# Kernel optimization log

Measured on AMD Instinct MI355X. Metric: run time of the kernel, lower is better.

The kernel has to match this reference:

```python
import jax, jax.numpy as jnp
import numpy as np

RADIUS, HMIN, HMAX, NSAMPLE = 0.05, -0.02, 0.04, 32
EPS = 1e-5


def setup_inputs() -> dict:
    key = jax.random.key(0)
    ks = jax.random.split(key, 6)
    B, N, C, OUT = 4, 2048, 256, 256
    seed_xyz_graspable = jax.random.uniform(ks[0], (B, N, 3), jnp.float32) * 0.2
    seed_features_graspable = jax.random.normal(ks[1], (B, C, N), jnp.float32)
    vp_rot = jax.random.normal(ks[2], (B, N, 3, 3), jnp.float32)
    W1 = jax.random.normal(ks[3], (OUT, 3 + C), jnp.float32) * 0.02
    W2 = jax.random.normal(ks[4], (OUT, OUT), jnp.float32) * 0.02
    return {
        "seed_xyz_graspable": seed_xyz_graspable,
        "seed_features_graspable": seed_features_graspable,
        "vp_rot": vp_rot,
        "W1": W1, "gamma1": jnp.ones((OUT,), jnp.float32), "beta1": jnp.zeros((OUT,), jnp.float32),
        "W2": W2, "gamma2": jnp.ones((OUT,), jnp.float32), "beta2": jnp.zeros((OUT,), jnp.float32),
    }


def _cylinder_query(xyz, rot):
    # xyz: (B,N,3), rot: (B,N,3,3); new_xyz == xyz.
    B, N, _ = xyz.shape
    d = xyz[:, None, :, :] - xyz[:, :, None, :]                  # (B,P,N,3) offsets to each candidate
    r = jnp.einsum('bpij,bpnj->bpni', rot, d)                    # rotate into cylinder frame (rot @ d)
    mask = (r[..., 1] ** 2 + r[..., 2] ** 2 < RADIUS ** 2) & (r[..., 0] > HMIN) & (r[..., 0] < HMAX)
    order = jnp.arange(N, dtype=jnp.int32)
    keys = jnp.where(mask, order, order + N)                     # in-cylinder points sort first, stable order
    _, idx = jax.lax.top_k(-keys, NSAMPLE)                       # first NSAMPLE indices satisfying the query
    valid = jnp.take_along_axis(mask, idx, axis=-1)
    first = idx[..., :1]
    any_valid = valid[..., :1]
    idx = jnp.where(valid, idx, jnp.where(any_valid, first, 0))  # pad with first hit like the CUDA kernel
    return idx                                                   # (B,P,NSAMPLE) int32


def _group(xyz, features, rot, idx):
    gxyz = jax.vmap(lambda a, i: a[i])(xyz, idx)                 # (B,P,S,3)
    gxyz = (gxyz - xyz[:, :, None, :]) / RADIUS                  # center on query + normalize_xyz
    gxyz = jnp.einsum('bpsj,bpjk->bpsk', gxyz, rot)              # rotate_xyz: grouped_xyz @ rot
    gfeat = jax.vmap(lambda f, i: f[:, i])(features, idx)        # (B,C,P,S)
    return jnp.concatenate([gxyz.transpose(0, 3, 1, 2), gfeat], axis=1)  # (B,3+C,P,S)


def _conv_bn_relu(x, W, gamma, beta):
    y = jnp.einsum('oc,bcps->bops', W, x)                        # 1x1 conv, no bias (bn=True)
    mu = y.mean(axis=(0, 2, 3), keepdims=True)
    var = y.var(axis=(0, 2, 3), keepdims=True)
    y = (y - mu) * jax.lax.rsqrt(var + EPS)
    y = y * gamma[None, :, None, None] + beta[None, :, None, None]
    return jax.nn.relu(y)


def reference(seed_xyz_graspable, seed_features_graspable, vp_rot, W1, gamma1, beta1, W2, gamma2, beta2):
    idx = _cylinder_query(seed_xyz_graspable, vp_rot)
    g = _group(seed_xyz_graspable, seed_features_graspable, vp_rot, idx)
    h = _conv_bn_relu(g, W1, gamma1, beta1)
    h = _conv_bn_relu(h, W2, gamma2, beta2)
    return h.max(axis=3)                                         # maxpool over nsample -> (B,OUT,P)
```

## Files before the change

kernel.cpp:

```cpp
#include <hip/hip_runtime.h>

typedef unsigned short u16;
typedef unsigned int u32;
typedef __attribute__((ext_vector_type(8))) short bf16x8;
typedef __attribute__((ext_vector_type(4))) float f32x4;

#define NPTS 2048
#define CFEAT 256
#define NS 32
#define MTOT 262144
#define NBLK 4096
#define INV_N (1.0f/262144.0f)

__device__ __forceinline__ float bf2f(u16 u) {
    union { u32 i; float f; } v; v.i = ((u32)u) << 16; return v.f;
}
__device__ __forceinline__ u16 f2bf(float f) {
    union { float f; u32 i; } v; v.f = f;
    u32 i = v.i;
    return (u16)((i + 0x7fffu + ((i >> 16) & 1u)) >> 16);
}

__global__ __launch_bounds__(256) void prep_k(const float* __restrict__ W1, const float* __restrict__ W2,
                                              u16* __restrict__ Wp1, u16* __restrict__ Wp2) {
    int o = blockIdx.x, t = threadIdx.x;
    Wp1[o * 288 + t] = f2bf(W1[o * 259 + 3 + t]);
    if (t < 32) Wp1[o * 288 + 256 + t] = (t < 3) ? f2bf(W1[o * 259 + t]) : (u16)0;
    Wp2[o * 256 + t] = f2bf(W2[o * 256 + t]);
}

__global__ __launch_bounds__(256) void query_k(const float* __restrict__ xyz, const float* __restrict__ rot,
                                               int* __restrict__ idx) {
    int pid = blockIdx.x * 4 + (threadIdx.x >> 6);
    int lane = threadIdx.x & 63;
    int b = pid >> 11, p = pid & 2047;
    const float* xb = xyz + (size_t)b * NPTS * 3;
    float px = xb[p * 3 + 0], py = xb[p * 3 + 1], pz = xb[p * 3 + 2];
    const float* rp = rot + (size_t)pid * 9;
    float r00 = rp[0], r01 = rp[1], r02 = rp[2];
    float r10 = rp[3], r11 = rp[4], r12 = rp[5];
    float r20 = rp[6], r21 = rp[7], r22 = rp[8];
    int cnt = 0, first = 0;
    for (int n0 = 0; n0 < NPTS && cnt < NS; n0 += 64) {
        int n = n0 + lane;
        float dx = __fsub_rn(xb[n * 3 + 0], px);
        float dy = __fsub_rn(xb[n * 3 + 1], py);
        float dz = __fsub_rn(xb[n * 3 + 2], pz);
        float a0 = __fadd_rn(__fadd_rn(__fmul_rn(r00, dx), __fmul_rn(r01, dy)), __fmul_rn(r02, dz));
        float a1 = __fadd_rn(__fadd_rn(__fmul_rn(r10, dx), __fmul_rn(r11, dy)), __fmul_rn(r12, dz));
        float a2 = __fadd_rn(__fadd_rn(__fmul_rn(r20, dx), __fmul_rn(r21, dy)), __fmul_rn(r22, dz));
        float t2 = __fadd_rn(__fmul_rn(a1, a1), __fmul_rn(a2, a2));
        bool valid = (t2 < 0.0025f) && (a0 > -0.02f) && (a0 < 0.04f);
        unsigned long long bal = __ballot(valid);
        if (cnt == 0 && bal) first = n0 + __builtin_ctzll(bal);
        int rank = __builtin_popcountll(bal & ((1ull << lane) - 1ull));
        int slot = cnt + rank;
        if (valid && slot < NS) idx[(size_t)pid * NS + slot] = n;
        cnt += __builtin_popcountll(bal);
    }
    int filled = cnt < NS ? cnt : NS;
    if (lane >= filled && lane < NS) idx[(size_t)pid * NS + lane] = (cnt > 0) ? first : 0;
}

__global__ __launch_bounds__(256) void featT_k(const float* __restrict__ feat, u16* __restrict__ featT) {
    __shared__ float sm[32 * 33];
    int b = blockIdx.z;
    int n0 = blockIdx.x * 32, c0 = blockIdx.y * 32;
    int t = threadIdx.x, x = t & 31, y = t >> 5;
    #pragma unroll
    for (int rr = 0; rr < 4; rr++) {
        int c = c0 + y + rr * 8;
        sm[(y + rr * 8) * 33 + x] = feat[((size_t)(b * CFEAT + c)) * NPTS + n0 + x];
    }
    __syncthreads();
    #pragma unroll
    for (int rr = 0; rr < 4; rr++) {
        int n = n0 + y + rr * 8;
        featT[((size_t)(b * NPTS + n)) * CFEAT + c0 + x] = f2bf(sm[x * 33 + (y + rr * 8)]);
    }
}

__global__ __launch_bounds__(256) void gxyz_k(const float* __restrict__ xyz, const float* __restrict__ rot,
                                              const int* __restrict__ idx, u16* __restrict__ gxyz) {
    int m = blockIdx.x * 256 + threadIdx.x;
    int pid = m >> 5;
    int b = pid >> 11, p = pid & 2047;
    int i = idx[m];
    const float* xb = xyz + (size_t)b * NPTS * 3;
    float dx = (xb[i * 3 + 0] - xb[p * 3 + 0]) * 20.0f;
    float dy = (xb[i * 3 + 1] - xb[p * 3 + 1]) * 20.0f;
    float dz = (xb[i * 3 + 2] - xb[p * 3 + 2]) * 20.0f;
    const float* rp = rot + (size_t)pid * 9;
    float g0 = dx * rp[0] + dy * rp[3] + dz * rp[6];
    float g1 = dx * rp[1] + dy * rp[4] + dz * rp[7];
    float g2 = dx * rp[2] + dy * rp[5] + dz * rp[8];
    uint2 v;
    v.x = (u32)f2bf(g0) | ((u32)f2bf(g1) << 16);
    v.y = (u32)f2bf(g2);
    *(uint2*)(gxyz + (size_t)m * 4) = v;
}

template <int FULL, int STORE>
__global__ __launch_bounds__(256) void fused_k(
    const u16* __restrict__ featT, const u16* __restrict__ gxyz, const int* __restrict__ idx,
    const u16* __restrict__ Wp1, const u16* __restrict__ Wp2, const float* __restrict__ ab1,
    float* __restrict__ psum, float* __restrict__ psq,
    float* __restrict__ ymax, float* __restrict__ ymin, uint2* __restrict__ y1f)
{
    __shared__ __attribute__((aligned(16))) u16 As[64 * 32];
    __shared__ __attribute__((aligned(16))) u16 Bs[256 * 32];
    __shared__ __attribute__((aligned(16))) u16 y1s[FULL ? 64 * 264 : 16];
    __shared__ int rowbase_s[64];

    const int tid = threadIdx.x;
    const int lane = tid & 63, wave = tid >> 6;
    const int quad = lane >> 4, tl = lane & 15;
    const int bx = blockIdx.x;
    const int m0 = bx * 64;

    if (tid < 64) {
        int m = m0 + tid;
        int gi = idx[m];
        int b = m >> 16;
        rowbase_s[tid] = (b * NPTS + gi) * CFEAT;
    }
    __syncthreads();
    const int srow = tid >> 2, sc16 = tid & 3;
    const int abase = rowbase_s[srow] + sc16 * 8;

    f32x4 acc[4][4];
    #pragma unroll
    for (int i = 0; i < 4; i++)
        #pragma unroll
        for (int j = 0; j < 4; j++) acc[i][j] = (f32x4){0.f, 0.f, 0.f, 0.f};

    auto mfma_tile = [&](f32x4 (&ac)[4][4], const u16* a_lds, int a_stride) {
        bf16x8 af[4], bv[4];
        #pragma unroll
        for (int i = 0; i < 4; i++) af[i] = *(const bf16x8*)(a_lds + (i * 16 + tl) * a_stride + quad * 8);
        #pragma unroll
        for (int j = 0; j < 4; j++) bv[j] = *(const bf16x8*)(Bs + (wave * 64 + j * 16 + tl) * 32 + quad * 8);
        #pragma unroll
        for (int i = 0; i < 4; i++)
            #pragma unroll
            for (int j = 0; j < 4; j++)
                ac[i][j] = __builtin_amdgcn_mfma_f32_16x16x32_bf16(af[i], bv[j], ac[i][j], 0, 0, 0);
    };

    for (int ks = 0; ks < 8; ks++) {
        const int k0 = ks * 32;
        __syncthreads();
        *(uint4*)(As + srow * 32 + sc16 * 8) = *(const uint4*)(featT + abase + k0);
        #pragma unroll
        for (int q = 0; q < 4; q++) {
            int o = srow + q * 64;
            *(uint4*)(Bs + o * 32 + sc16 * 8) = *(const uint4*)(Wp1 + o * 288 + k0 + sc16 * 8);
        }
        __syncthreads();
        mfma_tile(acc, As, 32);
    }
    {
        __syncthreads();
        uint4 va = make_uint4(0, 0, 0, 0);
        if (sc16 == 0) {
            uint2 g2 = *(const uint2*)(gxyz + (size_t)(m0 + srow) * 4);
            va.x = g2.x; va.y = g2.y;
        }
        *(uint4*)(As + srow * 32 + sc16 * 8) = va;
        #pragma unroll
        for (int q = 0; q < 4; q++) {
            int o = srow + q * 64;
            *(uint4*)(Bs + o * 32 + sc16 * 8) = *(const uint4*)(Wp1 + o * 288 + 256 + sc16 * 8);
        }
        __syncthreads();
        mfma_tile(acc, As, 32);
    }

    if (!FULL) {
        #pragma unroll
        for (int j = 0; j < 4; j++) {
            float s = 0.f, q2 = 0.f;
            #pragma unroll
            for (int i = 0; i < 4; i++) {
                float v0 = acc[i][j][0], v1 = acc[i][j][1], v2 = acc[i][j][2], v3 = acc[i][j][3];
                if (STORE) {
                    u32 lo = (u32)f2bf(v0) | ((u32)f2bf(v1) << 16);
                    u32 hi = (u32)f2bf(v2) | ((u32)f2bf(v3) << 16);
                    y1f[((size_t)(bx * 4 + wave) * 16 + i * 4 + j) * 64 + lane] = make_uint2(lo, hi);
                    v0 = bf2f((u16)(lo & 0xffff)); v1 = bf2f((u16)(lo >> 16));
                    v2 = bf2f((u16)(hi & 0xffff)); v3 = bf2f((u16)(hi >> 16));
                }
                s += v0 + v1 + v2 + v3;
                q2 += v0 * v0 + v1 * v1 + v2 * v2 + v3 * v3;
            }
            s += __shfl_xor(s, 16); s += __shfl_xor(s, 32);
            q2 += __shfl_xor(q2, 16); q2 += __shfl_xor(q2, 32);
            if (quad == 0) {
                int col = wave * 64 + j * 16 + tl;
                psum[(size_t)col * NBLK + bx] = s;
                psq[(size_t)col * NBLK + bx] = q2;
            }
        }
        return;
    }

    #pragma unroll
    for (int j = 0; j < 4; j++) {
        int col = wave * 64 + j * 16 + tl;
        float a = ab1[col], bb = ab1[256 + col];
        #pragma unroll
        for (int i = 0; i < 4; i++)
            #pragma unroll
            for (int r = 0; r < 4; r++) {
                float v = fmaxf(fmaf(acc[i][j][r], a, bb), 0.f);
                y1s[(i * 16 + quad * 4 + r) * 264 + col] = f2bf(v);
            }
    }

    f32x4 acc2[4][4];
    #pragma unroll
    for (int i = 0; i < 4; i++)
        #pragma unroll
        for (int j = 0; j < 4; j++) acc2[i][j] = (f32x4){0.f, 0.f, 0.f, 0.f};
    for (int ks = 0; ks < 8; ks++) {
        const int k0 = ks * 32;
        __syncthreads();
        #pragma unroll
        for (int q = 0; q < 4; q++) {
            int o = srow + q * 64;
            *(uint4*)(Bs + o * 32 + sc16 * 8) = *(const uint4*)(Wp2 + o * 256 + k0 + sc16 * 8);
        }
        __syncthreads();
        mfma_tile(acc2, y1s + k0, 264);
    }

    #pragma unroll
    for (int j = 0; j < 4; j++) {
        int col = wave * 64 + j * 16 + tl;
        float s = 0.f, q2 = 0.f;
        float mx0 = -3.0e38f, mn0 = 3.0e38f, mx1 = -3.0e38f, mn1 = 3.0e38f;
        #pragma unroll
        for (int i = 0; i < 4; i++)
            #pragma unroll
            for (int r = 0; r < 4; r++) {
                float v = acc2[i][j][r];
                s += v; q2 += v * v;
                if (i < 2) { mx0 = fmaxf(mx0, v); mn0 = fminf(mn0, v); }
                else       { mx1 = fmaxf(mx1, v); mn1 = fminf(mn1, v); }
            }
        s += __shfl_xor(s, 16); s += __shfl_xor(s, 32);
        q2 += __shfl_xor(q2, 16); q2 += __shfl_xor(q2, 32);
        mx0 = fmaxf(mx0, __shfl_xor(mx0, 16)); mx0 = fmaxf(mx0, __shfl_xor(mx0, 32));
        mn0 = fminf(mn0, __shfl_xor(mn0, 16)); mn0 = fminf(mn0, __shfl_xor(mn0, 32));
        mx1 = fmaxf(mx1, __shfl_xor(mx1, 16)); mx1 = fmaxf(mx1, __shfl_xor(mx1, 32));
        mn1 = fminf(mn1, __shfl_xor(mn1, 16)); mn1 = fminf(mn1, __shfl_xor(mn1, 32));
        if (quad == 0) {
            psum[(size_t)col * NBLK + bx] = s;
            psq[(size_t)col * NBLK + bx] = q2;
            size_t p0 = (size_t)(bx * 2) * 256 + col;
            size_t p1 = (size_t)(bx * 2 + 1) * 256 + col;
            ymax[p0] = mx0; ymin[p0] = mn0;
            ymax[p1] = mx1; ymin[p1] = mn1;
        }
    }
}

__global__ __launch_bounds__(256) void fused2_k(
    const uint2* __restrict__ y1f, const u16* __restrict__ Wp2, const float* __restrict__ ab1,
    float* __restrict__ psum, float* __restrict__ psq,
    float* __restrict__ ymax, float* __restrict__ ymin)
{
    __shared__ __attribute__((aligned(16))) u16 Bs[256 * 32];
    __shared__ __attribute__((aligned(16))) u16 y1s[64 * 264];
    const int tid = threadIdx.x;
    const int lane = tid & 63, wave = tid >> 6;
    const int quad = lane >> 4, tl = lane & 15;
    const int bx = blockIdx.x;

    #pragma unroll
    for (int j = 0; j < 4; j++) {
        int col = wave * 64 + j * 16 + tl;
        float a = ab1[col], bb = ab1[256 + col];
        #pragma unroll
        for (int i = 0; i < 4; i++) {
            uint2 v = y1f[((size_t)(bx * 4 + wave) * 16 + i * 4 + j) * 64 + lane];
            float f0 = bf2f((u16)(v.x & 0xffff)), f1 = bf2f((u16)(v.x >> 16));
            float f2 = bf2f((u16)(v.y & 0xffff)), f3 = bf2f((u16)(v.y >> 16));
            int rb = (i * 16 + quad * 4) * 264 + col;
            y1s[rb] = f2bf(fmaxf(fmaf(f0, a, bb), 0.f));
            y1s[rb + 264] = f2bf(fmaxf(fmaf(f1, a, bb), 0.f));
            y1s[rb + 528] = f2bf(fmaxf(fmaf(f2, a, bb), 0.f));
            y1s[rb + 792] = f2bf(fmaxf(fmaf(f3, a, bb), 0.f));
        }
    }

    const int srow = tid >> 2, sc16 = tid & 3;
    f32x4 acc2[4][4];
    #pragma unroll
    for (int i = 0; i < 4; i++)
        #pragma unroll
        for (int j = 0; j < 4; j++) acc2[i][j] = (f32x4){0.f, 0.f, 0.f, 0.f};

    for (int ks = 0; ks < 8; ks++) {
        const int k0 = ks * 32;
        __syncthreads();
        #pragma unroll
        for (int q = 0; q < 4; q++) {
            int o = srow + q * 64;
            *(uint4*)(Bs + o * 32 + sc16 * 8) = *(const uint4*)(Wp2 + o * 256 + k0 + sc16 * 8);
        }
        __syncthreads();
        bf16x8 af[4], bv[4];
        #pragma unroll
        for (int i = 0; i < 4; i++) af[i] = *(const bf16x8*)(y1s + (i * 16 + tl) * 264 + k0 + quad * 8);
        #pragma unroll
        for (int j = 0; j < 4; j++) bv[j] = *(const bf16x8*)(Bs + (wave * 64 + j * 16 + tl) * 32 + quad * 8);
        #pragma unroll
        for (int i = 0; i < 4; i++)
            #pragma unroll
            for (int j = 0; j < 4; j++)
                acc2[i][j] = __builtin_amdgcn_mfma_f32_16x16x32_bf16(af[i], bv[j], acc2[i][j], 0, 0, 0);
    }

    #pragma unroll
    for (int j = 0; j < 4; j++) {
        int col = wave * 64 + j * 16 + tl;
        float s = 0.f, q2 = 0.f;
        float mx0 = -3.0e38f, mn0 = 3.0e38f, mx1 = -3.0e38f, mn1 = 3.0e38f;
        #pragma unroll
        for (int i = 0; i < 4; i++)
            #pragma unroll
            for (int r = 0; r < 4; r++) {
                float v = acc2[i][j][r];
                s += v; q2 += v * v;
                if (i < 2) { mx0 = fmaxf(mx0, v); mn0 = fminf(mn0, v); }
                else       { mx1 = fmaxf(mx1, v); mn1 = fminf(mn1, v); }
            }
        s += __shfl_xor(s, 16); s += __shfl_xor(s, 32);
        q2 += __shfl_xor(q2, 16); q2 += __shfl_xor(q2, 32);
        mx0 = fmaxf(mx0, __shfl_xor(mx0, 16)); mx0 = fmaxf(mx0, __shfl_xor(mx0, 32));
        mn0 = fminf(mn0, __shfl_xor(mn0, 16)); mn0 = fminf(mn0, __shfl_xor(mn0, 32));
        mx1 = fmaxf(mx1, __shfl_xor(mx1, 16)); mx1 = fmaxf(mx1, __shfl_xor(mx1, 32));
        mn1 = fminf(mn1, __shfl_xor(mn1, 16)); mn1 = fminf(mn1, __shfl_xor(mn1, 32));
        if (quad == 0) {
            psum[(size_t)col * NBLK + bx] = s;
            psq[(size_t)col * NBLK + bx] = q2;
            size_t p0 = (size_t)(bx * 2) * 256 + col;
            size_t p1 = (size_t)(bx * 2 + 1) * 256 + col;
            ymax[p0] = mx0; ymin[p0] = mn0;
            ymax[p1] = mx1; ymin[p1] = mn1;
        }
    }
}

__global__ __launch_bounds__(256) void reduce_k(const float* __restrict__ psum, const float* __restrict__ psq,
                                                const float* __restrict__ gamma, const float* __restrict__ beta,
                                                float* __restrict__ ab) {
    __shared__ float red[8];
    int c = blockIdx.x, t = threadIdx.x;
    float s = 0.f, q = 0.f;
    for (int k = t; k < NBLK; k += 256) { s += psum[(size_t)c * NBLK + k]; q += psq[(size_t)c * NBLK + k]; }
    #pragma unroll
    for (int o = 32; o >= 1; o >>= 1) { s += __shfl_xor(s, o); q += __shfl_xor(q, o); }
    int lane = t & 63, w = t >> 6;
    if (lane == 0) { red[w] = s; red[4 + w] = q; }
    __syncthreads();
    if (t == 0) {
        float S = red[0] + red[1] + red[2] + red[3];
        float Q = red[4] + red[5] + red[6] + red[7];
        float mu = S * INV_N;
        float var = Q * INV_N - mu * mu;
        float a = gamma[c] * rsqrtf(var + 1e-5f);
        ab[c] = a;
        ab[256 + c] = beta[c] - mu * a;
    }
}

__global__ __launch_bounds__(256) void final_k(const float* __restrict__ ymax, const float* __restrict__ ymin,
                                               const float* __restrict__ ab, float* __restrict__ out) {
    __shared__ float sm[32 * 33];
    int b = blockIdx.z;
    int n0 = blockIdx.x * 32, o0 = blockIdx.y * 32;
    int t = threadIdx.x, x = t & 31, y = t >> 5;
    #pragma unroll
    for (int rr = 0; rr < 4; rr++) {
        int n = n0 + y + rr * 8;
        int o = o0 + x;
        float a = ab[o], bb = ab[256 + o];
        size_t p = (size_t)(b * NPTS + n) * 256 + o;
        float v = (a >= 0.f) ? ymax[p] : ymin[p];
        sm[(y + rr * 8) * 33 + x] = fmaxf(fmaf(v, a, bb), 0.f);
    }
    __syncthreads();
    #pragma unroll
    for (int rr = 0; rr < 4; rr++)
        out[((size_t)(b * 256 + o0 + y + rr * 8)) * NPTS + n0 + x] = sm[x * 33 + (y + rr * 8)];
}

extern "C" void kernel_launch(void* const* d_in, const int* in_sizes, int n_in,
                              void* d_out, int out_size, void* d_ws, size_t ws_size,
                              hipStream_t stream) {
    const float* xyz    = (const float*)d_in[0];
    const float* feat   = (const float*)d_in[1];
    const float* rot    = (const float*)d_in[2];
    const float* W1     = (const float*)d_in[3];
    const float* gamma1 = (const float*)d_in[4];
    const float* beta1  = (const float*)d_in[5];
    const float* W2     = (const float*)d_in[6];
    const float* gamma2 = (const float*)d_in[7];
    const float* beta2  = (const float*)d_in[8];
    float* out = (float*)d_out;

    char* ws = (char*)d_ws;
    u16*   featT = (u16*)(ws + 0);
    int*   idx   = (int*)(ws + 4194304);
    u16*   gxyz  = (u16*)(ws + 5242880);
    u16*   Wp1   = (u16*)(ws + 7340032);
    u16*   Wp2   = (u16*)(ws + 7487488);
    float* ab1   = (float*)(ws + 7618560);
    float* ab2   = (float*)(ws + 7620608);
    float* psum  = (float*)(ws + 7622656);
    float* psq   = (float*)(ws + 11816960);
    float* ymax  = (float*)(ws + 16011264);
    float* ymin  = (float*)(ws + 24399872);
    uint2* y1f   = (uint2*)(ws + 32788480);
    const size_t BIG_NEED = 32788480ull + 134217728ull;

    prep_k<<<256, 256, 0, stream>>>(W1, W2, Wp1, Wp2);
    query_k<<<2048, 256, 0, stream>>>(xyz, rot, idx);
    featT_k<<<dim3(64, 8, 4), 256, 0, stream>>>(feat, featT);
    gxyz_k<<<1024, 256, 0, stream>>>(xyz, rot, idx, gxyz);

    if (ws_size >= BIG_NEED) {
        fused_k<0, 1><<<NBLK, 256, 0, stream>>>(featT, gxyz, idx, Wp1, Wp2, ab1, psum, psq, ymax, ymin, y1f);
        reduce_k<<<256, 256, 0, stream>>>(psum, psq, gamma1, beta1, ab1);
        fused2_k<<<NBLK, 256, 0, stream>>>(y1f, Wp2, ab1, psum, psq, ymax, ymin);
        reduce_k<<<256, 256, 0, stream>>>(psum, psq, gamma2, beta2, ab2);
    } else {
        fused_k<0, 0><<<NBLK, 256, 0, stream>>>(featT, gxyz, idx, Wp1, Wp2, ab1, psum, psq, ymax, ymin, nullptr);
        reduce_k<<<256, 256, 0, stream>>>(psum, psq, gamma1, beta1, ab1);
        fused_k<1, 0><<<NBLK, 256, 0, stream>>>(featT, gxyz, idx, Wp1, Wp2, ab1, psum, psq, ymax, ymin, nullptr);
        reduce_k<<<256, 256, 0, stream>>>(psum, psq, gamma2, beta2, ab2);
    }
    final_k<<<dim3(64, 8, 4), 256, 0, stream>>>(ymax, ymin, ab2, out);
}
```

Baseline: 253.8 us.

## Use direct global-to-LDS loads and transpose partial-stat layout with two-stage reduce

Replaces register-staged global-to-shared copies of activation and weight tiles with global_load_lds direct-to-LDS transfers, which frees VGPRs and cuts instruction count in the GEMM loops. It also transposes the per-block BN partial sum layout to block-major, so the stores from each block are coalesced. The single strided reduction is replaced by a two-stage reduce (256 blocks, then 1 block). This adds an extra kernel launch and reuses workspace regions (ymin, gxyz) as scratch for the intermediate sums. The LDS write layout relies on the tid-linear mapping matching the original srow/sc16 layout.

```diff
diff --git a/kernel.cpp b/kernel.cpp
--- a/kernel.cpp
+++ b/kernel.cpp
@@ -19,6 +19,11 @@
     union { float f; u32 i; } v; v.f = f;
     u32 i = v.i;
     return (u16)((i + 0x7fffu + ((i >> 16) & 1u)) >> 16);
+}
+
+__device__ __forceinline__ void gload16(const void* g, void* l) {
+    __builtin_amdgcn_global_load_lds((const __attribute__((address_space(1))) void*)g,
+                                     (__attribute__((address_space(3))) void*)l, 16, 0, 0);
 }
 
 __global__ __launch_bounds__(256) void prep_k(const float* __restrict__ W1, const float* __restrict__ W2,
@@ -150,12 +155,10 @@
     for (int ks = 0; ks < 8; ks++) {
         const int k0 = ks * 32;
         __syncthreads();
-        *(uint4*)(As + srow * 32 + sc16 * 8) = *(const uint4*)(featT + abase + k0);
-        #pragma unroll
-        for (int q = 0; q < 4; q++) {
-            int o = srow + q * 64;
-            *(uint4*)(Bs + o * 32 + sc16 * 8) = *(const uint4*)(Wp1 + o * 288 + k0 + sc16 * 8);
-        }
+        gload16(featT + abase + k0, As + tid * 8);
+        #pragma unroll
+        for (int q = 0; q < 4; q++)
+            gload16(Wp1 + (srow + q * 64) * 288 + k0 + sc16 * 8, Bs + q * 2048 + tid * 8);
         __syncthreads();
         mfma_tile(acc, As, 32);
     }
@@ -168,10 +171,8 @@
         }
         *(uint4*)(As + srow * 32 + sc16 * 8) = va;
         #pragma unroll
-        for (int q = 0; q < 4; q++) {
-            int o = srow + q * 64;
-            *(uint4*)(Bs + o * 32 + sc16 * 8) = *(const uint4*)(Wp1 + o * 288 + 256 + sc16 * 8);
-        }
+        for (int q = 0; q < 4; q++)
+            gload16(Wp1 + (srow + q * 64) * 288 + 256 + sc16 * 8, Bs + q * 2048 + tid * 8);
         __syncthreads();
         mfma_tile(acc, As, 32);
     }
@@ -197,8 +198,8 @@
             q2 += __shfl_xor(q2, 16); q2 += __shfl_xor(q2, 32);
             if (quad == 0) {
                 int col = wave * 64 + j * 16 + tl;
-                psum[(size_t)col * NBLK + bx] = s;
-                psq[(size_t)col * NBLK + bx] = q2;
+                psum[(size_t)bx * 256 + col] = s;
+                psq[(size_t)bx * 256 + col] = q2;
             }
         }
         return;
@@ -226,10 +227,8 @@
         const int k0 = ks * 32;
         __syncthreads();
         #pragma unroll
-        for (int q = 0; q < 4; q++) {
-            int o = srow + q * 64;
-            *(uint4*)(Bs + o * 32 + sc16 * 8) = *(const uint4*)(Wp2 + o * 256 + k0 + sc16 * 8);
-        }
+        for (int q = 0; q < 4; q++)
+            gload16(Wp2 + (srow + q * 64) * 256 + k0 + sc16 * 8, Bs + q * 2048 + tid * 8);
         __syncthreads();
         mfma_tile(acc2, y1s + k0, 264);
     }
@@ -255,8 +254,8 @@
         mx1 = fmaxf(mx1, __shfl_xor(mx1, 16)); mx1 = fmaxf(mx1, __shfl_xor(mx1, 32));
         mn1 = fminf(mn1, __shfl_xor(mn1, 16)); mn1 = fminf(mn1, __shfl_xor(mn1, 32));
         if (quad == 0) {
-            psum[(size_t)col * NBLK + bx] = s;
-            psq[(size_t)col * NBLK + bx] = q2;
+            psum[(size_t)bx * 256 + col] = s;
+            psq[(size_t)bx * 256 + col] = q2;
             size_t p0 = (size_t)(bx * 2) * 256 + col;
             size_t p1 = (size_t)(bx * 2 + 1) * 256 + col;
             ymax[p0] = mx0; ymin[p0] = mn0;
@@ -305,10 +304,8 @@
         const int k0 = ks * 32;
         __syncthreads();
         #pragma unroll
-        for (int q = 0; q < 4; q++) {
-            int o = srow + q * 64;
-            *(uint4*)(Bs + o * 32 + sc16 * 8) = *(const uint4*)(Wp2 + o * 256 + k0 + sc16 * 8);
-        }
+        for (int q = 0; q < 4; q++)
+            gload16(Wp2 + (srow + q * 64) * 256 + k0 + sc16 * 8, Bs + q * 2048 + tid * 8);
         __syncthreads();
         bf16x8 af[4], bv[4];
         #pragma unroll
@@ -343,8 +340,8 @@
         mx1 = fmaxf(mx1, __shfl_xor(mx1, 16)); mx1 = fmaxf(mx1, __shfl_xor(mx1, 32));
         mn1 = fminf(mn1, __shfl_xor(mn1, 16)); mn1 = fminf(mn1, __shfl_xor(mn1, 32));
         if (quad == 0) {
-            psum[(size_t)col * NBLK + bx] = s;
-            psq[(size_t)col * NBLK + bx] = q2;
+            psum[(size_t)bx * 256 + col] = s;
+            psq[(size_t)bx * 256 + col] = q2;
             size_t p0 = (size_t)(bx * 2) * 256 + col;
             size_t p1 = (size_t)(bx * 2 + 1) * 256 + col;
             ymax[p0] = mx0; ymin[p0] = mn0;
@@ -353,27 +350,33 @@
     }
 }
 
-__global__ __launch_bounds__(256) void reduce_k(const float* __restrict__ psum, const float* __restrict__ psq,
-                                                const float* __restrict__ gamma, const float* __restrict__ beta,
-                                                float* __restrict__ ab) {
-    __shared__ float red[8];
-    int c = blockIdx.x, t = threadIdx.x;
+__global__ __launch_bounds__(256) void reduce1_k(const float* __restrict__ psum, const float* __restrict__ psq,
+                                                 float* __restrict__ ps2, float* __restrict__ pq2) {
+    int j = blockIdx.x, t = threadIdx.x;
     float s = 0.f, q = 0.f;
-    for (int k = t; k < NBLK; k += 256) { s += psum[(size_t)c * NBLK + k]; q += psq[(size_t)c * NBLK + k]; }
-    #pragma unroll
-    for (int o = 32; o >= 1; o >>= 1) { s += __shfl_xor(s, o); q += __shfl_xor(q, o); }
-    int lane = t & 63, w = t >> 6;
-    if (lane == 0) { red[w] = s; red[4 + w] = q; }
-    __syncthreads();
-    if (t == 0) {
-        float S = red[0] + red[1] + red[2] + red[3];
-        float Q = red[4] + red[5] + red[6] + red[7];
-        float mu = S * INV_N;
-        float var = Q * INV_N - mu * mu;
-        float a = gamma[c] * rsqrtf(var + 1e-5f);
-        ab[c] = a;
-        ab[256 + c] = beta[c] - mu * a;
-    }
+    #pragma unroll 4
+    for (int kk = 0; kk < 16; kk++) {
+        size_t r = (size_t)(j * 16 + kk) * 256 + t;
+        s += psum[r]; q += psq[r];
+    }
+    ps2[j * 256 + t] = s;
+    pq2[j * 256 + t] = q;
+}
+
+__global__ __launch_bounds__(256) void reduce2_k(const float* __restrict__ ps2, const float* __restrict__ pq2,
+                                                 const float* __restrict__ gamma, const float* __restrict__ beta,
+                                                 float* __restrict__ ab) {
+    int c = threadIdx.x;
+    float S = 0.f, Q = 0.f;
+    for (int j = 0; j < 256; j++) {
+        S += ps2[j * 256 + c];
+        Q += pq2[j * 256 + c];
+    }
+    float mu = S * INV_N;
+    float var = Q * INV_N - mu * mu;
+    float a = gamma[c] * rsqrtf(var + 1e-5f);
+    ab[c] = a;
+    ab[256 + c] = beta[c] - mu * a;
 }
 
 __global__ __launch_bounds__(256) void final_k(const float* __restrict__ ymax, const float* __restrict__ ymin,
@@ -426,6 +429,11 @@
     uint2* y1f   = (uint2*)(ws + 32788480);
     const size_t BIG_NEED = 32788480ull + 134217728ull;
 
+    float* r1s = (float*)(ws + 24399872);
+    float* r1q = r1s + 65536;
+    float* r2s = (float*)(ws + 5242880);
+    float* r2q = r2s + 65536;
+
     prep_k<<<256, 256, 0, stream>>>(W1, W2, Wp1, Wp2);
     query_k<<<2048, 256, 0, stream>>>(xyz, rot, idx);
     featT_k<<<dim3(64, 8, 4), 256, 0, stream>>>(feat, featT);
@@ -433,14 +441,18 @@
 
     if (ws_size >= BIG_NEED) {
         fused_k<0, 1><<<NBLK, 256, 0, stream>>>(featT, gxyz, idx, Wp1, Wp2, ab1, psum, psq, ymax, ymin, y1f);
-        reduce_k<<<256, 256, 0, stream>>>(psum, psq, gamma1, beta1, ab1);
+        reduce1_k<<<256, 256, 0, stream>>>(psum, psq, r1s, r1q);
+        reduce2_k<<<1, 256, 0, stream>>>(r1s, r1q, gamma1, beta1, ab1);
         fused2_k<<<NBLK, 256, 0, stream>>>(y1f, Wp2, ab1, psum, psq, ymax, ymin);
-        reduce_k<<<256, 256, 0, stream>>>(psum, psq, gamma2, beta2, ab2);
+        reduce1_k<<<256, 256, 0, stream>>>(psum, psq, r2s, r2q);
+        reduce2_k<<<1, 256, 0, stream>>>(r2s, r2q, gamma2, beta2, ab2);
     } else {
         fused_k<0, 0><<<NBLK, 256, 0, stream>>>(featT, gxyz, idx, Wp1, Wp2, ab1, psum, psq, ymax, ymin, nullptr);
-        reduce_k<<<256, 256, 0, stream>>>(psum, psq, gamma1, beta1, ab1);
+        reduce1_k<<<256, 256, 0, stream>>>(psum, psq, r1s, r1q);
+        reduce2_k<<<1, 256, 0, stream>>>(r1s, r1q, gamma1, beta1, ab1);
         fused_k<1, 0><<<NBLK, 256, 0, stream>>>(featT, gxyz, idx, Wp1, Wp2, ab1, psum, psq, ymax, ymin, nullptr);
-        reduce_k<<<256, 256, 0, stream>>>(psum, psq, gamma2, beta2, ab2);
+        reduce1_k<<<256, 256, 0, stream>>>(psum, psq, r2s, r2q);
+        reduce2_k<<<1, 256, 0, stream>>>(r2s, r2q, gamma2, beta2, ab2);
     }
     final_k<<<dim3(64, 8, 4), 256, 0, stream>>>(ymax, ymin, ab2, out);
 }
```

After: 258.2 us. About the same (+1.7%).
